# Kernel optimization log

Measured on AMD Instinct MI355X. Metric: run time of the kernel, lower is better.

The kernel has to match this reference:

```python
import jax, jax.numpy as jnp
import numpy as np

B, H, S, D = 4, 16, 2048, 64
TEMPERATURE = 8.0  # sqrt(d_k)
NEG_INF = -1e9


def setup_inputs() -> dict:
    key = jax.random.key(0)
    kq, kk, kv, kb = jax.random.split(key, 4)
    q = jax.random.normal(kq, (B, H, S, D), dtype=jnp.float32)
    k = jax.random.normal(kk, (B, H, S, D), dtype=jnp.float32)
    v = jax.random.normal(kv, (B, H, S, D), dtype=jnp.float32)
    mask = jnp.ones((B, 1, S, S), dtype=jnp.int32)
    attn_bias = jax.random.normal(kb, (B, H, S, S), dtype=jnp.float32)
    return {"q": q, "k": k, "v": v, "mask": mask, "attn_bias": attn_bias}


def reference(q, k, v, mask, attn_bias):
    # scores: [B,H,S,S]
    attn = jnp.einsum("bhqd,bhkd->bhqk", q / TEMPERATURE, k)
    attn = jnp.where(mask == 0, NEG_INF, attn)
    attn = attn + attn_bias
    # dropout p=0.0 -> identity
    norm_attn = jax.nn.softmax(attn, axis=-1)
    output = jnp.einsum("bhqk,bhkd->bhqd", norm_attn, v)
    return (output, attn)
```

## Files before the change

kernel.cpp:

```cpp
#include <hip/hip_runtime.h>
#include <math.h>

#define NBATCH 4
#define NHEAD  16
#define SEQ    2048
#define HDIM   64
#define QT     64
#define KT     64
#define NTILE  (SEQ / KT)
#define PSHIFT 8.0f

using f4v = __attribute__((ext_vector_type(4))) float;
using i4v = __attribute__((ext_vector_type(4))) int;
using h4  = __attribute__((ext_vector_type(4))) _Float16;
using h8  = __attribute__((ext_vector_type(8))) _Float16;

__device__ __forceinline__ void lds_barrier() {
    asm volatile("s_waitcnt lgkmcnt(0)" ::: "memory");
    __builtin_amdgcn_s_barrier();
}

__global__ __launch_bounds__(256) void fused_attn_v15(
    const float* __restrict__ qp, const float* __restrict__ kp,
    const float* __restrict__ vp, const int* __restrict__ maskp,
    const float* __restrict__ biasp, float* __restrict__ outp,
    float* __restrict__ attnp)
{
    __shared__ _Float16 s_tile[QT][72];
    __shared__ _Float16 ksh[2][KT][72];
    __shared__ _Float16 vsT[2][HDIM][72];

    const int t    = threadIdx.x;
    const int w    = t >> 6;
    const int lane = t & 63;
    const int g    = lane >> 4;
    const int r    = lane & 15;

    const int bh = blockIdx.y;
    const int b  = bh >> 4;
    const int q0 = blockIdx.x * QT;

    const int r0 = 16 * w + 4 * g;
    const int c0 = r << 2;

    const float* qg    = qp    + ((size_t)bh * SEQ + q0) * HDIM;
    const float* kg    = kp    + (size_t)bh * SEQ * HDIM;
    const float* vg    = vp    + (size_t)bh * SEQ * HDIM;
    const float* biasg = biasp + ((size_t)bh * SEQ + q0) * SEQ;
    const int*   maskg = maskp + ((size_t)b  * SEQ + q0) * SEQ;
    float*       attng = attnp + ((size_t)bh * SEQ + q0) * SEQ;
    float*       outg  = outp  + ((size_t)bh * SEQ + q0) * HDIM;

    h8 qf[2];
    {
        const float* p8 = qg + (16 * w + r) * HDIM;
        #pragma unroll
        for (int s = 0; s < 2; ++s) {
            f4v lo = *reinterpret_cast<const f4v*>(p8 + 32 * s + 8 * g);
            f4v hi = *reinterpret_cast<const f4v*>(p8 + 32 * s + 8 * g + 4);
            #pragma unroll
            for (int j = 0; j < 4; ++j) {
                qf[s][j]     = (_Float16)(0.125f * lo[j]);
                qf[s][j + 4] = (_Float16)(0.125f * hi[j]);
            }
        }
    }

    f4v  oacc[4];
    float l_i[4];
    #pragma unroll
    for (int i = 0; i < 4; ++i) { oacc[i] = (f4v){0.f,0.f,0.f,0.f}; l_i[i] = 0.f; }

    f4v   kreg[4];
    float vreg[16];

    auto issue_loads = [&](int tt) {
        const int k0 = tt * KT;
        #pragma unroll
        for (int it = 0; it < 4; ++it) {
            int i   = t + (it << 8);
            int key = i >> 4;
            int c4  = (i & 15) << 2;
            kreg[it] = *reinterpret_cast<const f4v*>(kg + (size_t)(k0 + key) * HDIM + c4);
        }
        #pragma unroll
        for (int it = 0; it < 4; ++it) {
            int kb = 4 * it + w;
            #pragma unroll
            for (int j = 0; j < 4; ++j)
                vreg[4 * it + j] = vg[(size_t)(k0 + 4 * kb + j) * HDIM + lane];
        }
    };

    auto write_stage = [&](int buf) {
        #pragma unroll
        for (int it = 0; it < 4; ++it) {
            int i   = t + (it << 8);
            int key = i >> 4;
            int c4  = (i & 15) << 2;
            h4 kh = { (_Float16)kreg[it][0], (_Float16)kreg[it][1],
                      (_Float16)kreg[it][2], (_Float16)kreg[it][3] };
            *reinterpret_cast<h4*>(&ksh[buf][key][c4]) = kh;
        }
        #pragma unroll
        for (int it = 0; it < 4; ++it) {
            int kb = 4 * it + w;
            h4 vh = { (_Float16)vreg[4*it+0], (_Float16)vreg[4*it+1],
                      (_Float16)vreg[4*it+2], (_Float16)vreg[4*it+3] };
            *reinterpret_cast<h4*>(&vsT[buf][lane][4 * kb]) = vh;
        }
    };

    auto issue_bm = [&](int tt, f4v* bv, i4v* mv) {
        const int k0 = tt * KT;
        #pragma unroll
        for (int i = 0; i < 4; ++i) {
            size_t rowoff = (size_t)(r0 + i) * SEQ + k0 + c0;
            mv[i] = *reinterpret_cast<const i4v*>(maskg + rowoff);
            bv[i] = *reinterpret_cast<const f4v*>(biasg + rowoff);
        }
    };

    auto compute = [&](int tt, int buf, f4v* bvC, i4v* mvC) {
        const int k0 = tt * KT;
        f4v acc[4];
        #pragma unroll
        for (int tc = 0; tc < 4; ++tc) acc[tc] = (f4v){0.f,0.f,0.f,0.f};
        #pragma unroll
        for (int tc = 0; tc < 4; ++tc) {
            #pragma unroll
            for (int s = 0; s < 2; ++s) {
                h8 kf = *reinterpret_cast<const h8*>(&ksh[buf][16 * tc + r][32 * s + 8 * g]);
                acc[tc] = __builtin_amdgcn_mfma_f32_16x16x32_f16(qf[s], kf, acc[tc], 0, 0, 0);
            }
        }
        #pragma unroll
        for (int tc = 0; tc < 4; ++tc) {
            #pragma unroll
            for (int j = 0; j < 4; ++j)
                s_tile[r0 + j][16 * tc + r] = (_Float16)acc[tc][j];
        }
        #pragma unroll
        for (int i = 0; i < 4; ++i) {
            size_t rowoff = (size_t)(r0 + i) * SEQ + k0 + c0;
            h4 sh = *reinterpret_cast<const h4*>(&s_tile[r0 + i][c0]);
            f4v sc;
            #pragma unroll
            for (int j = 0; j < 4; ++j)
                sc[j] = (mvC[i][j] == 0 ? -1e9f : (float)sh[j]) + bvC[i][j];
            *reinterpret_cast<f4v*>(attng + rowoff) = sc;
            f4v p;
            #pragma unroll
            for (int j = 0; j < 4; ++j) { p[j] = __expf(sc[j] - PSHIFT); l_i[i] += p[j]; }
            h4 ph = { (_Float16)p[0], (_Float16)p[1], (_Float16)p[2], (_Float16)p[3] };
            *reinterpret_cast<h4*>(&s_tile[r0 + i][c0]) = ph;
        }
        #pragma unroll
        for (int s = 0; s < 2; ++s) {
            h8 pf = *reinterpret_cast<const h8*>(&s_tile[16 * w + r][32 * s + 8 * g]);
            #pragma unroll
            for (int tc = 0; tc < 4; ++tc) {
                h8 vf = *reinterpret_cast<const h8*>(&vsT[buf][16 * tc + r][32 * s + 8 * g]);
                oacc[tc] = __builtin_amdgcn_mfma_f32_16x16x32_f16(pf, vf, oacc[tc], 0, 0, 0);
            }
        }
    };

    f4v bA[4], bB[4]; i4v mA[4], mB[4];
    issue_loads(0);
    issue_bm(0, bA, mA);
    write_stage(0);
    lds_barrier();

    for (int t2 = 0; t2 < NTILE; t2 += 2) {
        {
            issue_loads(t2 + 1);
            issue_bm(t2 + 1, bB, mB);
            compute(t2, 0, bA, mA);
            write_stage(1);
            lds_barrier();
        }
        {
            const bool more = (t2 + 2 < NTILE);
            if (more) { issue_loads(t2 + 2); issue_bm(t2 + 2, bA, mA); }
            compute(t2 + 1, 1, bB, mB);
            if (more) write_stage(0);
            lds_barrier();
        }
    }

    #pragma unroll
    for (int i = 0; i < 4; ++i) {
        #pragma unroll
        for (int off = 1; off < 16; off <<= 1)
            l_i[i] += __shfl_xor(l_i[i], off);
    }
    #pragma unroll
    for (int jr = 0; jr < 4; ++jr) {
        float inv = 1.f / l_i[jr];
        #pragma unroll
        for (int tc = 0; tc < 4; ++tc)
            outg[(size_t)(r0 + jr) * HDIM + 16 * tc + r] = oacc[tc][jr] * inv;
    }
}

extern "C" void kernel_launch(void* const* d_in, const int* in_sizes, int n_in,
                              void* d_out, int out_size, void* d_ws, size_t ws_size,
                              hipStream_t stream) {
    const float* q    = (const float*)d_in[0];
    const float* k    = (const float*)d_in[1];
    const float* v    = (const float*)d_in[2];
    const int*   mask = (const int*)  d_in[3];
    const float* bias = (const float*)d_in[4];
    float* out  = (float*)d_out;
    float* attn = out + (size_t)NBATCH * NHEAD * SEQ * HDIM;

    dim3 grid(SEQ / QT, NBATCH * NHEAD);
    fused_attn_v15<<<grid, dim3(256), 0, stream>>>(q, k, v, mask, bias, out, attn);
}
```

Baseline: 565.1 us.

## Pre-convert K to fp16 and pre-transpose V into workspace before fused attention

Adds two pre-pass kernels: one converts K to fp16 and one converts V to fp16 and transposes it into a [d][seq] layout in the workspace. The main kernel then loads K and V tiles as 16-byte fp16 vectors straight into LDS, with no per-tile conversion or strided scalar V loads. It also deepens prefetch so K/V run two tiles ahead and bias/mask are issued after compute. The cost is two extra launches and an extra pass over K and V, which is small next to the bias/mask/attn traffic. A fallback to the old kernel remains when the workspace is too small.

```diff
diff --git a/kernel.cpp b/kernel.cpp
--- a/kernel.cpp
+++ b/kernel.cpp
@@ -20,7 +20,229 @@
     __builtin_amdgcn_s_barrier();
 }
 
-__global__ __launch_bounds__(256) void fused_attn_v15(
+__global__ __launch_bounds__(256) void cvt_k(const float* __restrict__ in,
+                                             _Float16* __restrict__ out) {
+    size_t i = ((size_t)blockIdx.x * 256 + threadIdx.x) * 8;
+    f4v a = *reinterpret_cast<const f4v*>(in + i);
+    f4v b = *reinterpret_cast<const f4v*>(in + i + 4);
+    h8 o = { (_Float16)a[0], (_Float16)a[1], (_Float16)a[2], (_Float16)a[3],
+             (_Float16)b[0], (_Float16)b[1], (_Float16)b[2], (_Float16)b[3] };
+    *reinterpret_cast<h8*>(out + i) = o;
+}
+
+__global__ __launch_bounds__(256) void xpose_v(const float* __restrict__ vin,
+                                               _Float16* __restrict__ vout) {
+    __shared__ _Float16 vls[256][72];
+    const int t  = threadIdx.x;
+    const int c  = blockIdx.x;
+    const int bh = blockIdx.y;
+    const float* src = vin + ((size_t)bh * SEQ + (size_t)c * 256) * HDIM;
+    #pragma unroll
+    for (int it = 0; it < 16; ++it) {
+        int i   = t + it * 256;
+        int key = i >> 4;
+        int d4  = (i & 15) << 2;
+        f4v x = *reinterpret_cast<const f4v*>(src + (size_t)key * HDIM + d4);
+        h4 hx = { (_Float16)x[0], (_Float16)x[1], (_Float16)x[2], (_Float16)x[3] };
+        *reinterpret_cast<h4*>(&vls[key][d4]) = hx;
+    }
+    __syncthreads();
+    _Float16* dst = vout + (size_t)bh * HDIM * SEQ + (size_t)c * 256;
+    #pragma unroll
+    for (int it = 0; it < 8; ++it) {
+        int u  = t + it * 256;
+        int d  = u >> 5;
+        int k8 = (u & 31) << 3;
+        h8 o;
+        #pragma unroll
+        for (int j = 0; j < 8; ++j) o[j] = vls[k8 + j][d];
+        *reinterpret_cast<h8*>(dst + (size_t)d * SEQ + k8) = o;
+    }
+}
+
+__global__ __launch_bounds__(256) void fused_attn_v17(
+    const float* __restrict__ qp, const _Float16* __restrict__ kf16,
+    const _Float16* __restrict__ vt16, const int* __restrict__ maskp,
+    const float* __restrict__ biasp, float* __restrict__ outp,
+    float* __restrict__ attnp)
+{
+    __shared__ _Float16 s_tile[QT][72];
+    __shared__ _Float16 ksh[2][KT][72];
+    __shared__ _Float16 vsT[2][HDIM][72];
+
+    const int t    = threadIdx.x;
+    const int w    = t >> 6;
+    const int lane = t & 63;
+    const int g    = lane >> 4;
+    const int r    = lane & 15;
+
+    const int bh = blockIdx.y;
+    const int b  = bh >> 4;
+    const int q0 = blockIdx.x * QT;
+
+    const int r0 = 16 * w + 4 * g;
+    const int c0 = r << 2;
+
+    const float*    qg    = qp    + ((size_t)bh * SEQ + q0) * HDIM;
+    const _Float16* kg16  = kf16  + (size_t)bh * SEQ * HDIM;
+    const _Float16* vtg   = vt16  + (size_t)bh * HDIM * SEQ;
+    const float*    biasg = biasp + ((size_t)bh * SEQ + q0) * SEQ;
+    const int*      maskg = maskp + ((size_t)b  * SEQ + q0) * SEQ;
+    float*          attng = attnp + ((size_t)bh * SEQ + q0) * SEQ;
+    float*          outg  = outp  + ((size_t)bh * SEQ + q0) * HDIM;
+
+    h8 qf[2];
+    {
+        const float* p8 = qg + (16 * w + r) * HDIM;
+        #pragma unroll
+        for (int s = 0; s < 2; ++s) {
+            f4v lo = *reinterpret_cast<const f4v*>(p8 + 32 * s + 8 * g);
+            f4v hi = *reinterpret_cast<const f4v*>(p8 + 32 * s + 8 * g + 4);
+            #pragma unroll
+            for (int j = 0; j < 4; ++j) {
+                qf[s][j]     = (_Float16)(0.125f * lo[j]);
+                qf[s][j + 4] = (_Float16)(0.125f * hi[j]);
+            }
+        }
+    }
+
+    f4v  oacc[4];
+    float l_i[4];
+    #pragma unroll
+    for (int i = 0; i < 4; ++i) { oacc[i] = (f4v){0.f,0.f,0.f,0.f}; l_i[i] = 0.f; }
+
+    h8 kstg[2][2], vstg[2][2];
+
+    auto issueKV = [&](int tt, int set) {
+        const int k0 = tt * KT;
+        #pragma unroll
+        for (int u = 0; u < 2; ++u) {
+            int i = t + (u << 8);
+            int row = i >> 3, col8 = (i & 7) << 3;
+            kstg[set][u] = *reinterpret_cast<const h8*>(kg16 + (size_t)(k0 + row) * HDIM + col8);
+        }
+        #pragma unroll
+        for (int u = 0; u < 2; ++u) {
+            int i = t + (u << 8);
+            int d = i >> 3, k8 = (i & 7) << 3;
+            vstg[set][u] = *reinterpret_cast<const h8*>(vtg + (size_t)d * SEQ + k0 + k8);
+        }
+    };
+
+    auto write_stage = [&](int buf, int set) {
+        #pragma unroll
+        for (int u = 0; u < 2; ++u) {
+            int i = t + (u << 8);
+            int row = i >> 3, col8 = (i & 7) << 3;
+            *reinterpret_cast<h8*>(&ksh[buf][row][col8]) = kstg[set][u];
+        }
+        #pragma unroll
+        for (int u = 0; u < 2; ++u) {
+            int i = t + (u << 8);
+            int d = i >> 3, k8 = (i & 7) << 3;
+            *reinterpret_cast<h8*>(&vsT[buf][d][k8]) = vstg[set][u];
+        }
+    };
+
+    auto issue_bm = [&](int tt, f4v* bv, i4v* mv) {
+        const int k0 = tt * KT;
+        #pragma unroll
+        for (int i = 0; i < 4; ++i) {
+            size_t rowoff = (size_t)(r0 + i) * SEQ + k0 + c0;
+            mv[i] = *reinterpret_cast<const i4v*>(maskg + rowoff);
+            bv[i] = *reinterpret_cast<const f4v*>(biasg + rowoff);
+        }
+    };
+
+    auto compute = [&](int tt, int buf, f4v* bvC, i4v* mvC) {
+        const int k0 = tt * KT;
+        f4v acc[4];
+        #pragma unroll
+        for (int tc = 0; tc < 4; ++tc) acc[tc] = (f4v){0.f,0.f,0.f,0.f};
+        #pragma unroll
+        for (int tc = 0; tc < 4; ++tc) {
+            #pragma unroll
+            for (int s = 0; s < 2; ++s) {
+                h8 kf = *reinterpret_cast<const h8*>(&ksh[buf][16 * tc + r][32 * s + 8 * g]);
+                acc[tc] = __builtin_amdgcn_mfma_f32_16x16x32_f16(qf[s], kf, acc[tc], 0, 0, 0);
+            }
+        }
+        #pragma unroll
+        for (int tc = 0; tc < 4; ++tc) {
+            #pragma unroll
+            for (int j = 0; j < 4; ++j)
+                s_tile[r0 + j][16 * tc + r] = (_Float16)acc[tc][j];
+        }
+        #pragma unroll
+        for (int i = 0; i < 4; ++i) {
+            size_t rowoff = (size_t)(r0 + i) * SEQ + k0 + c0;
+            h4 sh = *reinterpret_cast<const h4*>(&s_tile[r0 + i][c0]);
+            f4v sc;
+            #pragma unroll
+            for (int j = 0; j < 4; ++j)
+                sc[j] = (mvC[i][j] == 0 ? -1e9f : (float)sh[j]) + bvC[i][j];
+            *reinterpret_cast<f4v*>(attng + rowoff) = sc;
+            f4v p;
+            #pragma unroll
+            for (int j = 0; j < 4; ++j) { p[j] = __expf(sc[j] - PSHIFT); l_i[i] += p[j]; }
+            h4 ph = { (_Float16)p[0], (_Float16)p[1], (_Float16)p[2], (_Float16)p[3] };
+            *reinterpret_cast<h4*>(&s_tile[r0 + i][c0]) = ph;
+        }
+        #pragma unroll
+        for (int s = 0; s < 2; ++s) {
+            h8 pf = *reinterpret_cast<const h8*>(&s_tile[16 * w + r][32 * s + 8 * g]);
+            #pragma unroll
+            for (int tc = 0; tc < 4; ++tc) {
+                h8 vf = *reinterpret_cast<const h8*>(&vsT[buf][16 * tc + r][32 * s + 8 * g]);
+                oacc[tc] = __builtin_amdgcn_mfma_f32_16x16x32_f16(pf, vf, oacc[tc], 0, 0, 0);
+            }
+        }
+    };
+
+    f4v bA[4], bB[4]; i4v mA[4], mB[4];
+    issueKV(0, 0);
+    issueKV(1, 1);
+    issue_bm(0, bA, mA);
+    issue_bm(1, bB, mB);
+    write_stage(0, 0);
+    lds_barrier();
+
+    for (int t2 = 0; t2 < NTILE; t2 += 2) {
+        {
+            const bool more = (t2 + 2 < NTILE);
+            if (more) issueKV(t2 + 2, 0);
+            compute(t2, 0, bA, mA);
+            if (more) issue_bm(t2 + 2, bA, mA);
+            write_stage(1, 1);
+            lds_barrier();
+        }
+        {
+            const bool more3 = (t2 + 3 < NTILE);
+            const bool more2 = (t2 + 2 < NTILE);
+            if (more3) issueKV(t2 + 3, 1);
+            compute(t2 + 1, 1, bB, mB);
+            if (more3) issue_bm(t2 + 3, bB, mB);
+            if (more2) write_stage(0, 0);
+            lds_barrier();
+        }
+    }
+
+    #pragma unroll
+    for (int i = 0; i < 4; ++i) {
+        #pragma unroll
+        for (int off = 1; off < 16; off <<= 1)
+            l_i[i] += __shfl_xor(l_i[i], off);
+    }
+    #pragma unroll
+    for (int jr = 0; jr < 4; ++jr) {
+        float inv = 1.f / l_i[jr];
+        #pragma unroll
+        for (int tc = 0; tc < 4; ++tc)
+            outg[(size_t)(r0 + jr) * HDIM + 16 * tc + r] = oacc[tc][jr] * inv;
+    }
+}
+
+__global__ __launch_bounds__(256) void fused_attn_fb(
     const float* __restrict__ qp, const float* __restrict__ kp,
     const float* __restrict__ vp, const int* __restrict__ maskp,
     const float* __restrict__ biasp, float* __restrict__ outp,
@@ -35,11 +257,9 @@
     const int lane = t & 63;
     const int g    = lane >> 4;
     const int r    = lane & 15;
-
     const int bh = blockIdx.y;
     const int b  = bh >> 4;
     const int q0 = blockIdx.x * QT;
-
     const int r0 = 16 * w + 4 * g;
     const int c0 = r << 2;
 
@@ -65,22 +285,17 @@
             }
         }
     }
-
-    f4v  oacc[4];
-    float l_i[4];
+    f4v  oacc[4]; float l_i[4];
     #pragma unroll
     for (int i = 0; i < 4; ++i) { oacc[i] = (f4v){0.f,0.f,0.f,0.f}; l_i[i] = 0.f; }
-
-    f4v   kreg[4];
-    float vreg[16];
+    f4v kreg[4]; float vreg[16];
 
     auto issue_loads = [&](int tt) {
         const int k0 = tt * KT;
         #pragma unroll
         for (int it = 0; it < 4; ++it) {
-            int i   = t + (it << 8);
-            int key = i >> 4;
-            int c4  = (i & 15) << 2;
+            int i = t + (it << 8);
+            int key = i >> 4, c4 = (i & 15) << 2;
             kreg[it] = *reinterpret_cast<const f4v*>(kg + (size_t)(k0 + key) * HDIM + c4);
         }
         #pragma unroll
@@ -91,13 +306,11 @@
                 vreg[4 * it + j] = vg[(size_t)(k0 + 4 * kb + j) * HDIM + lane];
         }
     };
-
     auto write_stage = [&](int buf) {
         #pragma unroll
         for (int it = 0; it < 4; ++it) {
-            int i   = t + (it << 8);
-            int key = i >> 4;
-            int c4  = (i & 15) << 2;
+            int i = t + (it << 8);
+            int key = i >> 4, c4 = (i & 15) << 2;
             h4 kh = { (_Float16)kreg[it][0], (_Float16)kreg[it][1],
                       (_Float16)kreg[it][2], (_Float16)kreg[it][3] };
             *reinterpret_cast<h4*>(&ksh[buf][key][c4]) = kh;
@@ -110,7 +323,6 @@
             *reinterpret_cast<h4*>(&vsT[buf][lane][4 * kb]) = vh;
         }
     };
-
     auto issue_bm = [&](int tt, f4v* bv, i4v* mv) {
         const int k0 = tt * KT;
         #pragma unroll
@@ -120,7 +332,6 @@
             bv[i] = *reinterpret_cast<const f4v*>(biasg + rowoff);
         }
     };
-
     auto compute = [&](int tt, int buf, f4v* bvC, i4v* mvC) {
         const int k0 = tt * KT;
         f4v acc[4];
@@ -167,18 +378,12 @@
     };
 
     f4v bA[4], bB[4]; i4v mA[4], mB[4];
-    issue_loads(0);
-    issue_bm(0, bA, mA);
-    write_stage(0);
-    lds_barrier();
-
+    issue_loads(0); issue_bm(0, bA, mA); write_stage(0); lds_barrier();
     for (int t2 = 0; t2 < NTILE; t2 += 2) {
         {
-            issue_loads(t2 + 1);
-            issue_bm(t2 + 1, bB, mB);
+            issue_loads(t2 + 1); issue_bm(t2 + 1, bB, mB);
             compute(t2, 0, bA, mA);
-            write_stage(1);
-            lds_barrier();
+            write_stage(1); lds_barrier();
         }
         {
             const bool more = (t2 + 2 < NTILE);
@@ -188,7 +393,6 @@
             lds_barrier();
         }
     }
-
     #pragma unroll
     for (int i = 0; i < 4; ++i) {
         #pragma unroll
@@ -216,5 +420,14 @@
     float* attn = out + (size_t)NBATCH * NHEAD * SEQ * HDIM;
 
     dim3 grid(SEQ / QT, NBATCH * NHEAD);
-    fused_attn_v15<<<grid, dim3(256), 0, stream>>>(q, k, v, mask, bias, out, attn);
-}
+    const size_t kvbytes = (size_t)NBATCH * NHEAD * SEQ * HDIM * sizeof(_Float16);
+    if (ws_size >= 2 * kvbytes) {
+        _Float16* kf16 = (_Float16*)d_ws;
+        _Float16* vt16 = (_Float16*)((char*)d_ws + kvbytes);
+        cvt_k<<<dim3(4096), dim3(256), 0, stream>>>(k, kf16);
+        xpose_v<<<dim3(8, NBATCH * NHEAD), dim3(256), 0, stream>>>(v, vt16);
+        fused_attn_v17<<<grid, dim3(256), 0, stream>>>(q, kf16, vt16, mask, bias, out, attn);
+    } else {
+        fused_attn_fb<<<grid, dim3(256), 0, stream>>>(q, k, v, mask, bias, out, attn);
+    }
+}
```

After: 548.9 us. -2.9%, faster.
